# Optimization experiments

Hardware: AMD Instinct MI355X
Metric: run time of the kernel (lower is better)

## Reference

```python
import jax, jax.numpy as jnp
import numpy as np

N = 50000      # nodes
E = 800000     # edges
G = 256        # graphs in batch
D_IN = 128     # input_dim
H = 128        # node_hidden_dim
FC = 128       # fc_hidden_dim
OUT = 2        # out_dim
EPS = 1e-5


def _lin_init(key, fan_in, fan_out, bias=True):
    kw, kb = jax.random.split(key)
    w = jax.random.normal(kw, (fan_in, fan_out), jnp.float32) / np.sqrt(fan_in)
    if bias:
        b = jax.random.normal(kb, (fan_out,), jnp.float32) * 0.01
        return w, b
    return w


def setup_inputs() -> dict:
    key = jax.random.key(0)
    ks = jax.random.split(key, 16)
    x = jax.random.normal(ks[0], (N, D_IN), jnp.float32)
    edge_index = jax.random.randint(ks[1], (2, E), 0, N, jnp.int32)
    batch = jnp.sort(jax.random.randint(ks[2], (N,), 0, G, jnp.int32))
    edge_attr = jax.random.uniform(ks[3], (E, 1), jnp.float32)
    # GraphConv params: lin_rel (with bias) + lin_root (no bias)
    w_rel1, b_rel1 = _lin_init(ks[4], D_IN, H)
    w_root1 = _lin_init(ks[5], D_IN, H, bias=False)
    w_rel2, b_rel2 = _lin_init(ks[6], H, 2 * H)
    w_root2 = _lin_init(ks[7], H, 2 * H, bias=False)
    w_rel3, b_rel3 = _lin_init(ks[8], 2 * H, 3 * H)
    w_root3 = _lin_init(ks[9], 2 * H, 3 * H, bias=False)
    # BatchNorm affine params
    gamma1 = jnp.ones((H,), jnp.float32);      beta1 = jnp.zeros((H,), jnp.float32)
    gamma2 = jnp.ones((2 * H,), jnp.float32);  beta2 = jnp.zeros((2 * H,), jnp.float32)
    gamma3 = jnp.ones((3 * H,), jnp.float32);  beta3 = jnp.zeros((3 * H,), jnp.float32)
    # FC head: lin1 in = 3H+6H+9H = 18H
    w_lin1, b_lin1 = _lin_init(ks[10], 18 * H, FC)
    w_lin2, b_lin2 = _lin_init(ks[11], FC, OUT)
    w_lin3, b_lin3 = _lin_init(ks[12], OUT, OUT)
    return dict(x=x, edge_index=edge_index, batch=batch, edge_attr=edge_attr,
                w_rel1=w_rel1, b_rel1=b_rel1, w_root1=w_root1,
                w_rel2=w_rel2, b_rel2=b_rel2, w_root2=w_root2,
                w_rel3=w_rel3, b_rel3=b_rel3, w_root3=w_root3,
                gamma1=gamma1, beta1=beta1, gamma2=gamma2, beta2=beta2,
                gamma3=gamma3, beta3=beta3,
                w_lin1=w_lin1, b_lin1=b_lin1, w_lin2=w_lin2, b_lin2=b_lin2,
                w_lin3=w_lin3, b_lin3=b_lin3)


def _bn(h, gamma, beta):
    # training-mode BatchNorm1d over node axis
    mu = h.mean(0)
    var = h.var(0)
    return (h - mu) * jax.lax.rsqrt(var + EPS) * gamma + beta


def _gconv(h, src, dst, ew, w_rel, b_rel, w_root):
    # PyG GraphConv: lin_rel(sum_j ew_ij * x_j) + lin_root(x_i)
    agg = jax.ops.segment_sum(h[src] * ew[:, None], dst, num_segments=N)
    return agg @ w_rel + b_rel + h @ w_root


def _pool3(h, batch):
    # concat of global max / mean / add pooling per graph
    s = jax.ops.segment_sum(h, batch, num_segments=G)
    cnt = jax.ops.segment_sum(jnp.ones((h.shape[0], 1), h.dtype), batch, num_segments=G)
    mean = s / jnp.maximum(cnt, 1.0)
    m = jax.ops.segment_max(h, batch, num_segments=G)
    m = jnp.where(cnt > 0, m, 0.0)  # guard empty segments
    return jnp.concatenate([m, mean, s], axis=1)


def reference(x, edge_index, batch, edge_attr,
              w_rel1, b_rel1, w_root1, w_rel2, b_rel2, w_root2,
              w_rel3, b_rel3, w_root3,
              gamma1, beta1, gamma2, beta2, gamma3, beta3,
              w_lin1, b_lin1, w_lin2, b_lin2, w_lin3, b_lin3):
    ew = jnp.transpose(edge_attr, (1, 0))[0]            # [E]
    src, dst = edge_index[0], edge_index[1]
    h = _bn(jax.nn.leaky_relu(_gconv(x, src, dst, ew, w_rel1, b_rel1, w_root1)), gamma1, beta1)
    x1 = _pool3(h, batch)
    h = _bn(jax.nn.leaky_relu(_gconv(h, src, dst, ew, w_rel2, b_rel2, w_root2)), gamma2, beta2)
    x2 = _pool3(h, batch)
    h = _bn(jax.nn.leaky_relu(_gconv(h, src, dst, ew, w_rel3, b_rel3, w_root3)), gamma3, beta3)
    x3 = _pool3(h, batch)
    z = jnp.concatenate([x1, x2, x3], axis=1)           # [G, 18H]
    z = jax.nn.relu(z @ w_lin1 + b_lin1)                # dropout is identity in eval
    z = jax.nn.relu(z @ w_lin2 + b_lin2)
    return jax.nn.log_softmax(z @ w_lin3 + b_lin3, axis=-1)
```

## Files before the change

### kernel.cpp

```cpp
#include <hip/hip_runtime.h>
#include <cstdint>
#include <cstddef>

#define N_NODES 50000
#define M_PAD   50048
#define MB_TILES 391
#define N_EDGES 800000
#define N_GRAPH 256
#define Z_DIM   2304
#define NREP    16
#define POOL_TOT (N_GRAPH * (128 + 256 + 384))

static constexpr float LEAKY  = 0.01f;
static constexpr float BN_EPS = 1e-5f;

typedef short short8 __attribute__((ext_vector_type(8)));
typedef float floatx4 __attribute__((ext_vector_type(4)));
typedef const __attribute__((address_space(1))) unsigned int* gas_ptr;
typedef __attribute__((address_space(3))) unsigned int* las_ptr;
typedef unsigned long long ull;

__device__ __forceinline__ unsigned short f2b(float f) {
  union { float f; unsigned int u; } v; v.f = f;
  unsigned int u = v.u;
  unsigned int r = (u + 0x7FFFu + ((u >> 16) & 1u)) >> 16;
  return (unsigned short)r;
}
__device__ __forceinline__ float b2f(unsigned short h) {
  union { unsigned int u; float f; } v; v.u = ((unsigned int)h) << 16;
  return v.f;
}
__device__ __forceinline__ unsigned fkey(float x) {
  unsigned k = __float_as_uint(x);
  return k ^ ((k & 0x80000000u) ? 0xFFFFFFFFu : 0x80000000u);
}
__device__ __forceinline__ float kdec(unsigned k) {
  k ^= (k & 0x80000000u) ? 0x80000000u : 0xFFFFFFFFu;
  return __uint_as_float(k);
}


__global__ void init_all_kernel(int* __restrict__ cntR, int* __restrict__ gcnt,
                                float* __restrict__ sums_all,
                                unsigned* __restrict__ pmaxk, unsigned* __restrict__ pmink,
                                float* __restrict__ psumg) {
  const int i = blockIdx.x * blockDim.x + threadIdx.x;
  if (i < NREP * N_NODES) cntR[i] = 0;
  if (i < N_GRAPH) gcnt[i] = 0;
  if (i < 2 * (128 + 256 + 384)) sums_all[i] = 0.f;
  if (i < POOL_TOT) { pmaxk[i] = 0u; pmink[i] = 0xFFFFFFFFu; psumg[i] = 0.f; }
}


__global__ void hist_rep_kernel(const int* __restrict__ idx, int* __restrict__ cntR, int n) {
  int i = blockIdx.x * blockDim.x + threadIdx.x;
  if (i < n) {
    const int rep = blockIdx.x & (NREP - 1);
    atomicAdd(&cntR[rep * N_NODES + idx[i]], 1);
  }
}

__global__ void combine_kernel(int* __restrict__ cntR, int* __restrict__ deg, int n) {
  int d = blockIdx.x * blockDim.x + threadIdx.x;
  if (d >= n) return;
  int s = 0;
#pragma unroll
  for (int r = 0; r < NREP; ++r) {
    const int c = cntR[r * N_NODES + d];
    cntR[r * N_NODES + d] = s;
    s += c;
  }
  deg[d] = s;
}

__global__ __launch_bounds__(256) void scan1_kernel(const int* __restrict__ in,
                                                    int* __restrict__ out,
                                                    int* __restrict__ part, int n) {
  __shared__ int sm[256];
  const int t = threadIdx.x;
  const int base = blockIdx.x * 1024 + t * 4;
  int v0 = 0, v1 = 0, v2 = 0, v3 = 0;
  if (base + 3 < n) {
    int4 q = *(const int4*)(in + base);
    v0 = q.x; v1 = q.y; v2 = q.z; v3 = q.w;
  } else {
    if (base     < n) v0 = in[base];
    if (base + 1 < n) v1 = in[base + 1];
    if (base + 2 < n) v2 = in[base + 2];
  }
  const int tsum = v0 + v1 + v2 + v3;
  sm[t] = tsum;
  __syncthreads();
  for (int off = 1; off < 256; off <<= 1) {
    int x = (t >= off) ? sm[t - off] : 0;
    __syncthreads();
    sm[t] += x;
    __syncthreads();
  }
  const int excl = sm[t] - tsum;
  if (base     < n) out[base]     = excl;
  if (base + 1 < n) out[base + 1] = excl + v0;
  if (base + 2 < n) out[base + 2] = excl + v0 + v1;
  if (base + 3 < n) out[base + 3] = excl + v0 + v1 + v2;
  if (t == 255) part[blockIdx.x] = sm[255];
}

__global__ __launch_bounds__(256) void scan2_kernel(int* __restrict__ part, int nb,
                                                    int* __restrict__ total_out) {
  __shared__ int sm[256];
  const int t = threadIdx.x;
  const int v = (t < nb) ? part[t] : 0;
  sm[t] = v;
  __syncthreads();
  for (int off = 1; off < 256; off <<= 1) {
    int x = (t >= off) ? sm[t - off] : 0;
    __syncthreads();
    sm[t] += x;
    __syncthreads();
  }
  if (t < nb) part[t] = sm[t] - v;
  if (t == 255) *total_out = sm[255];
}

__global__ void scan3_cursor_kernel(int* __restrict__ out, const int* __restrict__ part,
                                    int* __restrict__ cntR, int n) {
  int i = blockIdx.x * blockDim.x + threadIdx.x;
  if (i >= n) return;
  const int rp = out[i] + part[i >> 10];
  out[i] = rp;
#pragma unroll
  for (int r = 0; r < NREP; ++r) cntR[r * N_NODES + i] += rp;
}

__global__ void bucket_kernel(const int* __restrict__ src, const int* __restrict__ dst,
                              const float* __restrict__ ew, int* __restrict__ cntR,
                              ull* __restrict__ epack, int E) {
  int e = blockIdx.x * blockDim.x + threadIdx.x;
  if (e < E) {
    const int rep = blockIdx.x & (NREP - 1);
    const int d = dst[e];
    const int p = atomicAdd(&cntR[rep * N_NODES + d], 1);
    epack[p] = ((ull)__float_as_uint(ew[e]) << 32) | (unsigned)src[e];
  }
}

__global__ __launch_bounds__(256) void hist_batch_kernel(const int* __restrict__ idx,
                                                         int* __restrict__ cnt, int n) {
  __shared__ int lh[N_GRAPH];
  lh[threadIdx.x] = 0;
  __syncthreads();
  int i = blockIdx.x * blockDim.x + threadIdx.x;
  if (i < n) atomicAdd(&lh[idx[i]], 1);
  __syncthreads();
  const int v = lh[threadIdx.x];
  if (v) atomicAdd(&cnt[threadIdx.x], v);
}

__global__ __launch_bounds__(256) void scan256_kernel(const int* __restrict__ cnt,
                                                      int* __restrict__ gptr) {
  __shared__ int sm[256];
  const int t = threadIdx.x;
  const int v = cnt[t];
  sm[t] = v;
  __syncthreads();
  for (int off = 1; off < 256; off <<= 1) {
    int x = (t >= off) ? sm[t - off] : 0;
    __syncthreads();
    sm[t] += x;
    __syncthreads();
  }
  gptr[t] = sm[t] - v;
  if (t == 255) gptr[256] = sm[255];
}


__global__ void cast_bf16_kernel(const float* __restrict__ in,
                                 unsigned short* __restrict__ out, int npair) {
  int i = blockIdx.x * blockDim.x + threadIdx.x;
  if (i >= npair) return;
  float2 v = *(const float2*)(in + 2 * (size_t)i);
  ((unsigned int*)out)[i] = (unsigned int)f2b(v.x) | ((unsigned int)f2b(v.y) << 16);
}

__global__ __launch_bounds__(256) void wt_build_kernel(
    const float* __restrict__ wrel, const float* __restrict__ wroot,
    const float* __restrict__ brel, const float* __restrict__ sums_prev,
    const float* __restrict__ gamma_prev, const float* __restrict__ beta_prev,
    unsigned short* __restrict__ wt, float* __restrict__ u, float* __restrict__ v,
    int K, int N) {
  __shared__ float redu[256];
  __shared__ float redv[256];
  const int n = blockIdx.x;
  const int K2 = 2 * K;
  const float inv_n = 1.f / (float)N_NODES;
  float us = 0.f, vs = 0.f;
  for (int k = threadIdx.x; k < K2; k += 256) {
    const int kk = (k < K) ? k : k - K;
    const float w = (k < K) ? wrel[(size_t)kk * N + n] : wroot[(size_t)kk * N + n];
    float sc = 1.f, sh = 0.f;
    if (sums_prev) {
      const float mu  = sums_prev[kk] * inv_n;
      const float var = sums_prev[K + kk] * inv_n - mu * mu;
      sc = rsqrtf(var + BN_EPS) * gamma_prev[kk];
      sh = beta_prev[kk] - mu * sc;
    }
    wt[(size_t)n * K2 + k] = f2b(w * sc);
    if (k < K) us += sh * w; else vs += sh * w;
  }
  redu[threadIdx.x] = us; redv[threadIdx.x] = vs;
  __syncthreads();
  for (int o = 128; o > 0; o >>= 1) {
    if (threadIdx.x < o) {
      redu[threadIdx.x] += redu[threadIdx.x + o];
      redv[threadIdx.x] += redv[threadIdx.x + o];
    }
    __syncthreads();
  }
  if (threadIdx.x == 0) { u[n] = redu[0]; v[n] = brel[n] + redv[0]; }
}


template <int D>
__global__ void agg_bf16_kernel(const unsigned short* __restrict__ h,
                                const int* __restrict__ rowptr,
                                const ull* __restrict__ epack,
                                unsigned short* __restrict__ agg,
                                float* __restrict__ degw_out) {
  int gid  = blockIdx.x * blockDim.x + threadIdx.x;
  int node = gid >> 6;
  int lane = threadIdx.x & 63;
  if (node >= N_NODES) return;
  const int beg = rowptr[node], end = rowptr[node + 1];
  constexpr int NP = D / 128;
  float acc0[NP], acc1[NP];
#pragma unroll
  for (int i = 0; i < NP; ++i) { acc0[i] = 0.f; acc1[i] = 0.f; }
  float wsum = 0.f;

  int p = beg;
  for (; p + 4 <= end; p += 4) {
    const ull p0 = epack[p],     p1 = epack[p + 1];
    const ull p2 = epack[p + 2], p3 = epack[p + 3];
    const int s0 = (int)(unsigned)p0, s1 = (int)(unsigned)p1;
    const int s2 = (int)(unsigned)p2, s3 = (int)(unsigned)p3;
    const float w0 = __uint_as_float((unsigned)(p0 >> 32));
    const float w1 = __uint_as_float((unsigned)(p1 >> 32));
    const float w2 = __uint_as_float((unsigned)(p2 >> 32));
    const float w3 = __uint_as_float((unsigned)(p3 >> 32));
    wsum += w0 + w1 + w2 + w3;
    const unsigned int* r0 = (const unsigned int*)(h + (size_t)s0 * D);
    const unsigned int* r1 = (const unsigned int*)(h + (size_t)s1 * D);
    const unsigned int* r2 = (const unsigned int*)(h + (size_t)s2 * D);
    const unsigned int* r3 = (const unsigned int*)(h + (size_t)s3 * D);
    unsigned int u0[NP], u1[NP], u2[NP], u3[NP];
#pragma unroll
    for (int i = 0; i < NP; ++i) {
      u0[i] = r0[lane + 64 * i];
      u1[i] = r1[lane + 64 * i];
      u2[i] = r2[lane + 64 * i];
      u3[i] = r3[lane + 64 * i];
    }
#pragma unroll
    for (int i = 0; i < NP; ++i) {
      acc0[i] += b2f((unsigned short)(u0[i] & 0xFFFF)) * w0
               + b2f((unsigned short)(u1[i] & 0xFFFF)) * w1
               + b2f((unsigned short)(u2[i] & 0xFFFF)) * w2
               + b2f((unsigned short)(u3[i] & 0xFFFF)) * w3;
      acc1[i] += b2f((unsigned short)(u0[i] >> 16)) * w0
               + b2f((unsigned short)(u1[i] >> 16)) * w1
               + b2f((unsigned short)(u2[i] >> 16)) * w2
               + b2f((unsigned short)(u3[i] >> 16)) * w3;
    }
  }
  for (; p < end; ++p) {
    const ull pk = epack[p];
    const int   s = (int)(unsigned)pk;
    const float w = __uint_as_float((unsigned)(pk >> 32));
    wsum += w;
    const unsigned int* row = (const unsigned int*)(h + (size_t)s * D);
#pragma unroll
    for (int i = 0; i < NP; ++i) {
      unsigned int uu = row[lane + 64 * i];
      acc0[i] += b2f((unsigned short)(uu & 0xFFFF)) * w;
      acc1[i] += b2f((unsigned short)(uu >> 16)) * w;
    }
  }
  unsigned int* o = (unsigned int*)(agg + (size_t)node * D);
#pragma unroll
  for (int i = 0; i < NP; ++i)
    o[lane + 64 * i] = (unsigned int)f2b(acc0[i]) | ((unsigned int)f2b(acc1[i]) << 16);
  if (degw_out != nullptr && lane == 0) degw_out[node] = wsum;
}


__global__ __launch_bounds__(256) void gemm_mfma_kernel(
    const unsigned short* __restrict__ Aagg, const unsigned short* __restrict__ Ah,
    const unsigned short* __restrict__ Wt,
    const float* __restrict__ u, const float* __restrict__ v,
    const float* __restrict__ degw,
    unsigned short* __restrict__ outH, float* __restrict__ sums,
    int M, int K, int N) {
  __shared__ unsigned short As[2][128 * 32];
  __shared__ unsigned short Bs[2][128 * 32];
  __shared__ float col_s[256];
  __shared__ float dws[128];

  const int NT = N >> 7;
  const int id = blockIdx.x;
  const int xcd = id & 7;
  const int q   = id >> 3;
  const int m_tile = (q / NT) * 8 + xcd;
  if (m_tile >= MB_TILES) return;
  const int m0 = m_tile * 128;
  const int n0 = (q % NT) * 128;

  const int t  = threadIdx.x;
  const int lane = t & 63;
  const int w    = t >> 6;
  const int wm   = (w & 1) * 64;
  const int wn   = (w >> 1) * 64;
  const int l16  = lane & 15;
  const int lq   = lane >> 4;
  const int K2   = 2 * K;

  const int lrow  = lane >> 2;
  const int lslot = lane & 3;

  col_s[t] = 0.f;
  if (t < 128) {
    const int m = m0 + t;
    dws[t] = (m < M) ? degw[m] : 0.f;
  }

  floatx4 acc[4][4];
#pragma unroll
  for (int i = 0; i < 4; ++i)
#pragma unroll
    for (int j = 0; j < 4; ++j) acc[i][j] = (floatx4){0.f, 0.f, 0.f, 0.f};

  for (int k0 = 0; k0 < K2; k0 += 64) {
    __syncthreads();
#pragma unroll
    for (int h = 0; h < 2; ++h) {
      const int kk = k0 + h * 32;
      const unsigned short* Asrc;
      int kbase;
      if (kk < K) { Asrc = Aagg; kbase = kk; } else { Asrc = Ah; kbase = kk - K; }
#pragma unroll
      for (int qq = 0; qq < 2; ++qq) {
        const int row = w * 32 + qq * 16 + lrow;
        const int gc  = (lslot ^ ((row >> 1) & 3)) * 8;
        const unsigned short* gA = Asrc + (size_t)(m0 + row) * K + kbase + gc;
        const unsigned short* gB = Wt + (size_t)(n0 + row) * K2 + kk + gc;
        __builtin_amdgcn_global_load_lds((gas_ptr)gA,
                                         (las_ptr)(As[h] + (w * 32 + qq * 16) * 32), 16, 0, 0);
        __builtin_amdgcn_global_load_lds((gas_ptr)gB,
                                         (las_ptr)(Bs[h] + (w * 32 + qq * 16) * 32), 16, 0, 0);
      }
    }
    __syncthreads();

#pragma unroll
    for (int h = 0; h < 2; ++h) {
      short8 af[4], bfr[4];
#pragma unroll
      for (int i = 0; i < 4; ++i) {
        const int r = wm + i * 16 + l16;
        af[i] = *(const short8*)(As[h] + r * 32 + (lq ^ ((r >> 1) & 3)) * 8);
      }
#pragma unroll
      for (int j = 0; j < 4; ++j) {
        const int r = wn + j * 16 + l16;
        bfr[j] = *(const short8*)(Bs[h] + r * 32 + (lq ^ ((r >> 1) & 3)) * 8);
      }
#pragma unroll
      for (int i = 0; i < 4; ++i)
#pragma unroll
        for (int j = 0; j < 4; ++j)
          acc[i][j] = __builtin_amdgcn_mfma_f32_16x16x32_bf16(af[i], bfr[j], acc[i][j], 0, 0, 0);
    }
  }

  float uu[4], vv[4];
#pragma unroll
  for (int j = 0; j < 4; ++j) {
    const int n = n0 + wn + j * 16 + l16;
    uu[j] = u[n]; vv[j] = v[n];
  }

  float ts[4]  = {0.f, 0.f, 0.f, 0.f};
  float tss[4] = {0.f, 0.f, 0.f, 0.f};
#pragma unroll
  for (int i = 0; i < 4; ++i) {
    const int lrow2 = wm + i * 16 + lq * 4;
#pragma unroll
    for (int j = 0; j < 4; ++j) {
      const int n = n0 + wn + j * 16 + l16;
#pragma unroll
      for (int r = 0; r < 4; ++r) {
        const int m = m0 + lrow2 + r;
        if (m < M) {
          float val = acc[i][j][r] + vv[j] + dws[lrow2 + r] * uu[j];
          val = val > 0.f ? val : LEAKY * val;
          outH[(size_t)m * N + n] = f2b(val);
          ts[j]  += val;
          tss[j] += val * val;
        }
      }
    }
  }
#pragma unroll
  for (int j = 0; j < 4; ++j) {
    float a = ts[j], b = tss[j];
    a += __shfl_xor(a, 16); a += __shfl_xor(a, 32);
    b += __shfl_xor(b, 16); b += __shfl_xor(b, 32);
    if (lq == 0) {
      const int ci = wn + j * 16 + l16;
      atomicAdd(&col_s[ci], a);
      atomicAdd(&col_s[128 + ci], b);
    }
  }
  __syncthreads();
  if (t < 128) {
    atomicAdd(&sums[n0 + t], col_s[t]);
    atomicAdd(&sums[N + n0 + t], col_s[128 + t]);
  }
}


__global__ void pool_bf16_kernel(const unsigned short* __restrict__ hp,
                                 const int* __restrict__ batch,
                                 unsigned* __restrict__ pmaxk, unsigned* __restrict__ pmink,
                                 float* __restrict__ psumg, int n, int C) {
  __shared__ int bs[64];
  const int tc = threadIdx.x;
  const int r0 = blockIdx.x * 64;
  const int r1 = min(n, r0 + 64);
  if (tc < 64 && r0 + tc < n) bs[tc] = batch[r0 + tc];
  __syncthreads();
  int cur_g = bs[0];
  float mx0 = -3.4e38f, mn0 = 3.4e38f, s0 = 0.f;
  float mx1 = -3.4e38f, mn1 = 3.4e38f, s1 = 0.f;
  for (int r = r0; r < r1; ++r) {
    const int g = bs[r - r0];
    if (g != cur_g) {
      const int c0 = 2 * tc;
      atomicMax(&pmaxk[(size_t)cur_g * C + c0], fkey(mx0));
      atomicMin(&pmink[(size_t)cur_g * C + c0], fkey(mn0));
      atomicAdd(&psumg[(size_t)cur_g * C + c0], s0);
      atomicMax(&pmaxk[(size_t)cur_g * C + c0 + 1], fkey(mx1));
      atomicMin(&pmink[(size_t)cur_g * C + c0 + 1], fkey(mn1));
      atomicAdd(&psumg[(size_t)cur_g * C + c0 + 1], s1);
      mx0 = -3.4e38f; mn0 = 3.4e38f; s0 = 0.f;
      mx1 = -3.4e38f; mn1 = 3.4e38f; s1 = 0.f;
      cur_g = g;
    }
    const unsigned uu = ((const unsigned*)(hp + (size_t)r * C))[tc];
    const float a = b2f((unsigned short)(uu & 0xFFFF));
    const float b = b2f((unsigned short)(uu >> 16));
    mx0 = fmaxf(mx0, a); mn0 = fminf(mn0, a); s0 += a;
    mx1 = fmaxf(mx1, b); mn1 = fminf(mn1, b); s1 += b;
  }
  const int c0 = 2 * tc;
  atomicMax(&pmaxk[(size_t)cur_g * C + c0], fkey(mx0));
  atomicMin(&pmink[(size_t)cur_g * C + c0], fkey(mn0));
  atomicAdd(&psumg[(size_t)cur_g * C + c0], s0);
  atomicMax(&pmaxk[(size_t)cur_g * C + c0 + 1], fkey(mx1));
  atomicMin(&pmink[(size_t)cur_g * C + c0 + 1], fkey(mn1));
  atomicAdd(&psumg[(size_t)cur_g * C + c0 + 1], s1);
}


__global__ void pool_finalize_kernel(const unsigned* __restrict__ pmaxk,
                                     const unsigned* __restrict__ pmink,
                                     const float* __restrict__ psumg,
                                     const float* __restrict__ sums,
                                     const float* __restrict__ gamma,
                                     const float* __restrict__ beta,
                                     const int* __restrict__ gptr,
                                     float* __restrict__ z, int C, int zoff) {
  int i = blockIdx.x * blockDim.x + threadIdx.x;
  if (i >= N_GRAPH * C) return;
  const int g = i / C, c = i % C;
  const int cnt = gptr[g + 1] - gptr[g];
  const float inv_n = 1.f / (float)N_NODES;
  const float mu  = sums[c] * inv_n;
  const float var = sums[C + c] * inv_n - mu * mu;
  const float sc  = rsqrtf(var + BN_EPS) * gamma[c];
  const float sh  = beta[c] - mu * sc;
  const float mx = kdec(pmaxk[i]);
  const float mn = kdec(pmink[i]);
  const float sm = psumg[i];
  const float zmax = (sc >= 0.f ? mx : mn) * sc + sh;
  const float zsum = sm * sc + (float)cnt * sh;
  float* zg = z + (size_t)g * Z_DIM + zoff;
  zg[c]         = (cnt > 0) ? zmax : 0.f;
  zg[C + c]     = zsum / (float)(cnt > 0 ? cnt : 1);
  zg[2 * C + c] = zsum;
}


__global__ __launch_bounds__(1024) void fc_kernel(const float* __restrict__ z,
                                                  const float* __restrict__ w1, const float* __restrict__ b1,
                                                  const float* __restrict__ w2, const float* __restrict__ b2,
                                                  const float* __restrict__ w3, const float* __restrict__ b3,
                                                  float* __restrict__ out) {
  __shared__ float zs[Z_DIM];
  __shared__ float part[8][128];
  __shared__ float h1s[128];
  __shared__ float red[128][2];
  __shared__ float y2[2];
  const int g  = blockIdx.x;
  const int t  = threadIdx.x;
  const int c  = t & 127;
  const int ks = t >> 7;
  for (int i = t; i < Z_DIM; i += 1024) zs[i] = z[(size_t)g * Z_DIM + i];
  __syncthreads();

  constexpr int KCH = Z_DIM / 8;
  const int k0 = ks * KCH;
  float acc = 0.f;
#pragma unroll 4
  for (int k = k0; k < k0 + KCH; ++k) acc += zs[k] * w1[(size_t)k * 128 + c];
  part[ks][c] = acc;
  __syncthreads();

  if (t < 128) {
    float s = b1[t];
#pragma unroll
    for (int i = 0; i < 8; ++i) s += part[i][t];
    h1s[t] = fmaxf(s, 0.f);
  }
  __syncthreads();
  if (t < 128) {
    red[t][0] = h1s[t] * w2[t * 2 + 0];
    red[t][1] = h1s[t] * w2[t * 2 + 1];
  }
  __syncthreads();
  if (t < 2) {
    float s = b2[t];
    for (int k = 0; k < 128; ++k) s += red[k][t];
    y2[t] = fmaxf(s, 0.f);
  }
  __syncthreads();
  if (t == 0) {
    const float z0 = y2[0] * w3[0] + y2[1] * w3[2] + b3[0];
    const float z1 = y2[0] * w3[1] + y2[1] * w3[3] + b3[1];
    const float m  = fmaxf(z0, z1);
    const float lse = m + logf(expf(z0 - m) + expf(z1 - m));
    out[g * 2 + 0] = z0 - lse;
    out[g * 2 + 1] = z1 - lse;
  }
}


extern "C" void kernel_launch(void* const* d_in, const int* in_sizes, int n_in,
                              void* d_out, int out_size, void* d_ws, size_t ws_size,
                              hipStream_t stream) {
  (void)in_sizes; (void)n_in; (void)out_size; (void)ws_size;
  const float* x        = (const float*)d_in[0];
  const int*   eidx     = (const int*)d_in[1];
  const int*   batch    = (const int*)d_in[2];
  const float* eattr    = (const float*)d_in[3];
  const float* w_rel1   = (const float*)d_in[4];
  const float* b_rel1   = (const float*)d_in[5];
  const float* w_root1  = (const float*)d_in[6];
  const float* w_rel2   = (const float*)d_in[7];
  const float* b_rel2   = (const float*)d_in[8];
  const float* w_root2  = (const float*)d_in[9];
  const float* w_rel3   = (const float*)d_in[10];
  const float* b_rel3   = (const float*)d_in[11];
  const float* w_root3  = (const float*)d_in[12];
  const float* gamma1   = (const float*)d_in[13];
  const float* beta1    = (const float*)d_in[14];
  const float* gamma2   = (const float*)d_in[15];
  const float* beta2    = (const float*)d_in[16];
  const float* gamma3   = (const float*)d_in[17];
  const float* beta3    = (const float*)d_in[18];
  const float* w_lin1   = (const float*)d_in[19];
  const float* b_lin1   = (const float*)d_in[20];
  const float* w_lin2   = (const float*)d_in[21];
  const float* b_lin2   = (const float*)d_in[22];
  const float* w_lin3   = (const float*)d_in[23];
  const float* b_lin3   = (const float*)d_in[24];

  const int* src = eidx;
  const int* dst = eidx + N_EDGES;
  float* outp = (float*)d_out;

  char* ws = (char*)d_ws;
  size_t off = 0;
  auto alloc = [&](size_t bytes) -> void* {
    void* p = ws + off;
    off += (bytes + 255) & ~(size_t)255;
    return p;
  };
  int*   rowptr = (int*)alloc((N_NODES + 1) * sizeof(int));
  int*   deg    = (int*)alloc(N_NODES * sizeof(int));
  int*   cntR   = (int*)alloc((size_t)NREP * N_NODES * sizeof(int));
  int*   gptr   = (int*)alloc((N_GRAPH + 1) * sizeof(int));
  int*   gcnt   = (int*)alloc(N_GRAPH * sizeof(int));
  int*   part   = (int*)alloc(256 * sizeof(int));
  ull*   epack  = (ull*)alloc((size_t)N_EDGES * sizeof(ull));
  float* degw   = (float*)alloc(N_NODES * sizeof(float));
  float* sums_all = (float*)alloc(2 * (128 + 256 + 384) * sizeof(float));
  float* zbuf   = (float*)alloc((size_t)N_GRAPH * Z_DIM * sizeof(float));
  unsigned* pmaxk = (unsigned*)alloc((size_t)POOL_TOT * 4);
  unsigned* pmink = (unsigned*)alloc((size_t)POOL_TOT * 4);
  float*    psumg = (float*)alloc((size_t)POOL_TOT * 4);
  unsigned short* xb   = (unsigned short*)alloc((size_t)M_PAD * 128 * 2);
  unsigned short* hp1  = (unsigned short*)alloc((size_t)M_PAD * 128 * 2);
  unsigned short* hp2  = (unsigned short*)alloc((size_t)M_PAD * 256 * 2);
  unsigned short* hp3  = (unsigned short*)alloc((size_t)M_PAD * 384 * 2);
  unsigned short* aggb = (unsigned short*)alloc((size_t)M_PAD * 256 * 2);
  unsigned short* wt1 = (unsigned short*)alloc((size_t)128 * 256 * 2);
  unsigned short* wt2 = (unsigned short*)alloc((size_t)256 * 256 * 2);
  unsigned short* wt3 = (unsigned short*)alloc((size_t)384 * 512 * 2);
  float* u1 = (float*)alloc(128 * sizeof(float));
  float* v1 = (float*)alloc(128 * sizeof(float));
  float* u2 = (float*)alloc(256 * sizeof(float));
  float* v2 = (float*)alloc(256 * sizeof(float));
  float* u3 = (float*)alloc(384 * sizeof(float));
  float* v3 = (float*)alloc(384 * sizeof(float));

  float* sums1 = sums_all;
  float* sums2 = sums_all + 2 * 128;
  float* sums3 = sums_all + 2 * (128 + 256);
  const int PO1 = 0, PO2 = N_GRAPH * 128, PO3 = N_GRAPH * (128 + 256);

  const int EB = (N_EDGES + 255) / 256;
  const int NB = (N_NODES + 255) / 256;
  const int RB = (N_NODES + 63) / 64;
  const int SB = (N_NODES + 1023) / 1024;

  init_all_kernel<<<(NREP * N_NODES + 255) / 256, 256, 0, stream>>>(
      cntR, gcnt, sums_all, pmaxk, pmink, psumg);

  hist_rep_kernel<<<EB, 256, 0, stream>>>(dst, cntR, N_EDGES);
  combine_kernel<<<NB, 256, 0, stream>>>(cntR, deg, N_NODES);
  scan1_kernel<<<SB, 256, 0, stream>>>(deg, rowptr, part, N_NODES);
  scan2_kernel<<<1, 256, 0, stream>>>(part, SB, rowptr + N_NODES);
  scan3_cursor_kernel<<<NB, 256, 0, stream>>>(rowptr, part, cntR, N_NODES);
  bucket_kernel<<<EB, 256, 0, stream>>>(src, dst, eattr, cntR, epack, N_EDGES);

  hist_batch_kernel<<<NB, 256, 0, stream>>>(batch, gcnt, N_NODES);
  scan256_kernel<<<1, 256, 0, stream>>>(gcnt, gptr);

  cast_bf16_kernel<<<(N_NODES * 128 / 2 + 255) / 256, 256, 0, stream>>>(x, xb, N_NODES * 128 / 2);
  wt_build_kernel<<<128, 256, 0, stream>>>(w_rel1, w_root1, b_rel1, nullptr, nullptr, nullptr,
                                           wt1, u1, v1, 128, 128);

  const int aggBlocks = (N_NODES * 64 + 255) / 256;

  agg_bf16_kernel<128><<<aggBlocks, 256, 0, stream>>>(xb, rowptr, epack, aggb, degw);
  gemm_mfma_kernel<<<392 * 1, 256, 0, stream>>>(aggb, xb, wt1, u1, v1, degw,
                                                hp1, sums1, N_NODES, 128, 128);
  pool_bf16_kernel<<<RB, 64, 0, stream>>>(hp1, batch, pmaxk + PO1, pmink + PO1, psumg + PO1,
                                          N_NODES, 128);
  pool_finalize_kernel<<<(N_GRAPH * 128 + 255) / 256, 256, 0, stream>>>(
      pmaxk + PO1, pmink + PO1, psumg + PO1, sums1, gamma1, beta1, gptr, zbuf, 128, 0);
  wt_build_kernel<<<256, 256, 0, stream>>>(w_rel2, w_root2, b_rel2, sums1, gamma1, beta1,
                                           wt2, u2, v2, 128, 256);

  agg_bf16_kernel<128><<<aggBlocks, 256, 0, stream>>>(hp1, rowptr, epack, aggb, nullptr);
  gemm_mfma_kernel<<<392 * 2, 256, 0, stream>>>(aggb, hp1, wt2, u2, v2, degw,
                                                hp2, sums2, N_NODES, 128, 256);
  pool_bf16_kernel<<<RB, 128, 0, stream>>>(hp2, batch, pmaxk + PO2, pmink + PO2, psumg + PO2,
                                           N_NODES, 256);
  pool_finalize_kernel<<<(N_GRAPH * 256 + 255) / 256, 256, 0, stream>>>(
      pmaxk + PO2, pmink + PO2, psumg + PO2, sums2, gamma2, beta2, gptr, zbuf, 256, 384);
  wt_build_kernel<<<384, 256, 0, stream>>>(w_rel3, w_root3, b_rel3, sums2, gamma2, beta2,
                                           wt3, u3, v3, 256, 384);

  agg_bf16_kernel<256><<<aggBlocks, 256, 0, stream>>>(hp2, rowptr, epack, aggb, nullptr);
  gemm_mfma_kernel<<<392 * 3, 256, 0, stream>>>(aggb, hp2, wt3, u3, v3, degw,
                                                hp3, sums3, N_NODES, 256, 384);
  pool_bf16_kernel<<<RB, 192, 0, stream>>>(hp3, batch, pmaxk + PO3, pmink + PO3, psumg + PO3,
                                           N_NODES, 384);
  pool_finalize_kernel<<<(N_GRAPH * 384 + 255) / 256, 256, 0, stream>>>(
      pmaxk + PO3, pmink + PO3, psumg + PO3, sums3, gamma3, beta3, gptr, zbuf, 384, 1152);

  fc_kernel<<<N_GRAPH, 1024, 0, stream>>>(zbuf, w_lin1, b_lin1, w_lin2, b_lin2, w_lin3, b_lin3,
                                          outp);
}
```

Measured before the change: 582.2 us.

## Fuse degree combine into scan, merge pool finalizes, shrink GEMM K-step

Folds the per-replica degree combine into the first scan kernel and merges the three per-layer pool finalize launches into one launch at the end. Together these remove three kernel launches. Separately, the MFMA GEMM drops its two-half LDS buffers and iterates K in steps of 32 instead of 64. That halves LDS use, which may raise occupancy, but doubles the number of barriers per tile. The fused scan now does strided 16-way loads per element instead of a coalesced int4 read, which may cost memory efficiency.

```diff
diff --git a/kernel.cpp b/kernel.cpp
--- a/kernel.cpp
+++ b/kernel.cpp
@@ -60,35 +60,28 @@
   }
 }
 
-__global__ void combine_kernel(int* __restrict__ cntR, int* __restrict__ deg, int n) {
-  int d = blockIdx.x * blockDim.x + threadIdx.x;
-  if (d >= n) return;
-  int s = 0;
-#pragma unroll
-  for (int r = 0; r < NREP; ++r) {
-    const int c = cntR[r * N_NODES + d];
-    cntR[r * N_NODES + d] = s;
-    s += c;
-  }
-  deg[d] = s;
-}
-
-__global__ __launch_bounds__(256) void scan1_kernel(const int* __restrict__ in,
-                                                    int* __restrict__ out,
-                                                    int* __restrict__ part, int n) {
+__global__ __launch_bounds__(256) void scan1_fused_kernel(int* __restrict__ cntR,
+                                                          int* __restrict__ out,
+                                                          int* __restrict__ part, int n) {
   __shared__ int sm[256];
   const int t = threadIdx.x;
   const int base = blockIdx.x * 1024 + t * 4;
-  int v0 = 0, v1 = 0, v2 = 0, v3 = 0;
-  if (base + 3 < n) {
-    int4 q = *(const int4*)(in + base);
-    v0 = q.x; v1 = q.y; v2 = q.z; v3 = q.w;
-  } else {
-    if (base     < n) v0 = in[base];
-    if (base + 1 < n) v1 = in[base + 1];
-    if (base + 2 < n) v2 = in[base + 2];
-  }
-  const int tsum = v0 + v1 + v2 + v3;
+  int v[4] = {0, 0, 0, 0};
+#pragma unroll
+  for (int j = 0; j < 4; ++j) {
+    const int d = base + j;
+    if (d < n) {
+      int s = 0;
+#pragma unroll
+      for (int r = 0; r < NREP; ++r) {
+        const int c = cntR[r * N_NODES + d];
+        cntR[r * N_NODES + d] = s;
+        s += c;
+      }
+      v[j] = s;
+    }
+  }
+  const int tsum = v[0] + v[1] + v[2] + v[3];
   sm[t] = tsum;
   __syncthreads();
   for (int off = 1; off < 256; off <<= 1) {
@@ -99,9 +92,9 @@
   }
   const int excl = sm[t] - tsum;
   if (base     < n) out[base]     = excl;
-  if (base + 1 < n) out[base + 1] = excl + v0;
-  if (base + 2 < n) out[base + 2] = excl + v0 + v1;
-  if (base + 3 < n) out[base + 3] = excl + v0 + v1 + v2;
+  if (base + 1 < n) out[base + 1] = excl + v[0];
+  if (base + 2 < n) out[base + 2] = excl + v[0] + v[1];
+  if (base + 3 < n) out[base + 3] = excl + v[0] + v[1] + v[2];
   if (t == 255) part[blockIdx.x] = sm[255];
 }
 
@@ -300,8 +293,8 @@
     const float* __restrict__ degw,
     unsigned short* __restrict__ outH, float* __restrict__ sums,
     int M, int K, int N) {
-  __shared__ unsigned short As[2][128 * 32];
-  __shared__ unsigned short Bs[2][128 * 32];
+  __shared__ unsigned short As[128 * 32];
+  __shared__ unsigned short Bs[128 * 32];
   __shared__ float col_s[256];
   __shared__ float dws[128];
 
@@ -338,47 +331,42 @@
 #pragma unroll
     for (int j = 0; j < 4; ++j) acc[i][j] = (floatx4){0.f, 0.f, 0.f, 0.f};
 
-  for (int k0 = 0; k0 < K2; k0 += 64) {
-    __syncthreads();
-#pragma unroll
-    for (int h = 0; h < 2; ++h) {
-      const int kk = k0 + h * 32;
-      const unsigned short* Asrc;
-      int kbase;
-      if (kk < K) { Asrc = Aagg; kbase = kk; } else { Asrc = Ah; kbase = kk - K; }
-#pragma unroll
-      for (int qq = 0; qq < 2; ++qq) {
-        const int row = w * 32 + qq * 16 + lrow;
-        const int gc  = (lslot ^ ((row >> 1) & 3)) * 8;
-        const unsigned short* gA = Asrc + (size_t)(m0 + row) * K + kbase + gc;
-        const unsigned short* gB = Wt + (size_t)(n0 + row) * K2 + kk + gc;
-        __builtin_amdgcn_global_load_lds((gas_ptr)gA,
-                                         (las_ptr)(As[h] + (w * 32 + qq * 16) * 32), 16, 0, 0);
-        __builtin_amdgcn_global_load_lds((gas_ptr)gB,
-                                         (las_ptr)(Bs[h] + (w * 32 + qq * 16) * 32), 16, 0, 0);
-      }
-    }
-    __syncthreads();
-
-#pragma unroll
-    for (int h = 0; h < 2; ++h) {
-      short8 af[4], bfr[4];
-#pragma unroll
-      for (int i = 0; i < 4; ++i) {
-        const int r = wm + i * 16 + l16;
-        af[i] = *(const short8*)(As[h] + r * 32 + (lq ^ ((r >> 1) & 3)) * 8);
-      }
-#pragma unroll
-      for (int j = 0; j < 4; ++j) {
-        const int r = wn + j * 16 + l16;
-        bfr[j] = *(const short8*)(Bs[h] + r * 32 + (lq ^ ((r >> 1) & 3)) * 8);
-      }
-#pragma unroll
-      for (int i = 0; i < 4; ++i)
-#pragma unroll
-        for (int j = 0; j < 4; ++j)
-          acc[i][j] = __builtin_amdgcn_mfma_f32_16x16x32_bf16(af[i], bfr[j], acc[i][j], 0, 0, 0);
-    }
+  for (int k0 = 0; k0 < K2; k0 += 32) {
+    const unsigned short* Asrc;
+    int kbase;
+    if (k0 < K) { Asrc = Aagg; kbase = k0; } else { Asrc = Ah; kbase = k0 - K; }
+
+    __syncthreads();
+#pragma unroll
+    for (int qq = 0; qq < 2; ++qq) {
+      const int row = w * 32 + qq * 16 + lrow;
+      const int gc  = (lslot ^ ((row >> 1) & 3)) * 8;
+      const unsigned short* gA = Asrc + (size_t)(m0 + row) * K + kbase + gc;
+      const unsigned short* gB = Wt + (size_t)(n0 + row) * K2 + k0 + gc;
+      __builtin_amdgcn_global_load_lds((gas_ptr)gA, (las_ptr)(As + (w * 32 + qq * 16) * 32),
+                                       16, 0, 0);
+      __builtin_amdgcn_global_load_lds((gas_ptr)gB, (las_ptr)(Bs + (w * 32 + qq * 16) * 32),
+                                       16, 0, 0);
+    }
+    __syncthreads();
+
+    short8 af[4], bfr[4];
+#pragma unroll
+    for (int i = 0; i < 4; ++i) {
+      const int r = wm + i * 16 + l16;
+      af[i] = *(const short8*)(As + r * 32 + (lq ^ ((r >> 1) & 3)) * 8);
+    }
+#pragma unroll
+    for (int j = 0; j < 4; ++j) {
+      const int r = wn + j * 16 + l16;
+      bfr[j] = *(const short8*)(Bs + r * 32 + (lq ^ ((r >> 1) & 3)) * 8);
+    }
+
+#pragma unroll
+    for (int i = 0; i < 4; ++i)
+#pragma unroll
+      for (int j = 0; j < 4; ++j)
+        acc[i][j] = __builtin_amdgcn_mfma_f32_16x16x32_bf16(af[i], bfr[j], acc[i][j], 0, 0, 0);
   }
 
   float uu[4], vv[4];
@@ -471,17 +459,30 @@
 }
 
 
-__global__ void pool_finalize_kernel(const unsigned* __restrict__ pmaxk,
-                                     const unsigned* __restrict__ pmink,
-                                     const float* __restrict__ psumg,
-                                     const float* __restrict__ sums,
-                                     const float* __restrict__ gamma,
-                                     const float* __restrict__ beta,
-                                     const int* __restrict__ gptr,
-                                     float* __restrict__ z, int C, int zoff) {
+__global__ void pool_finalize_all_kernel(const unsigned* __restrict__ pmaxk,
+                                         const unsigned* __restrict__ pmink,
+                                         const float* __restrict__ psumg,
+                                         const float* __restrict__ sums_all,
+                                         const float* __restrict__ gamma1, const float* __restrict__ beta1,
+                                         const float* __restrict__ gamma2, const float* __restrict__ beta2,
+                                         const float* __restrict__ gamma3, const float* __restrict__ beta3,
+                                         const int* __restrict__ gptr,
+                                         float* __restrict__ z) {
   int i = blockIdx.x * blockDim.x + threadIdx.x;
-  if (i >= N_GRAPH * C) return;
-  const int g = i / C, c = i % C;
+  if (i >= POOL_TOT) return;
+  int C, zoff, li;
+  const float *sums, *gamma, *beta;
+  if (i < N_GRAPH * 128) {
+    C = 128; zoff = 0; li = i;
+    sums = sums_all; gamma = gamma1; beta = beta1;
+  } else if (i < N_GRAPH * (128 + 256)) {
+    C = 256; zoff = 384; li = i - N_GRAPH * 128;
+    sums = sums_all + 2 * 128; gamma = gamma2; beta = beta2;
+  } else {
+    C = 384; zoff = 1152; li = i - N_GRAPH * (128 + 256);
+    sums = sums_all + 2 * (128 + 256); gamma = gamma3; beta = beta3;
+  }
+  const int g = li / C, c = li % C;
   const int cnt = gptr[g + 1] - gptr[g];
   const float inv_n = 1.f / (float)N_NODES;
   const float mu  = sums[c] * inv_n;
@@ -596,7 +597,6 @@
     return p;
   };
   int*   rowptr = (int*)alloc((N_NODES + 1) * sizeof(int));
-  int*   deg    = (int*)alloc(N_NODES * sizeof(int));
   int*   cntR   = (int*)alloc((size_t)NREP * N_NODES * sizeof(int));
   int*   gptr   = (int*)alloc((N_GRAPH + 1) * sizeof(int));
   int*   gcnt   = (int*)alloc(N_GRAPH * sizeof(int));
@@ -637,8 +637,7 @@
       cntR, gcnt, sums_all, pmaxk, pmink, psumg);
 
   hist_rep_kernel<<<EB, 256, 0, stream>>>(dst, cntR, N_EDGES);
-  combine_kernel<<<NB, 256, 0, stream>>>(cntR, deg, N_NODES);
-  scan1_kernel<<<SB, 256, 0, stream>>>(deg, rowptr, part, N_NODES);
+  scan1_fused_kernel<<<SB, 256, 0, stream>>>(cntR, rowptr, part, N_NODES);
   scan2_kernel<<<1, 256, 0, stream>>>(part, SB, rowptr + N_NODES);
   scan3_cursor_kernel<<<NB, 256, 0, stream>>>(rowptr, part, cntR, N_NODES);
   bucket_kernel<<<EB, 256, 0, stream>>>(src, dst, eattr, cntR, epack, N_EDGES);
@@ -657,8 +656,6 @@
                                                 hp1, sums1, N_NODES, 128, 128);
   pool_bf16_kernel<<<RB, 64, 0, stream>>>(hp1, batch, pmaxk + PO1, pmink + PO1, psumg + PO1,
                                           N_NODES, 128);
-  pool_finalize_kernel<<<(N_GRAPH * 128 + 255) / 256, 256, 0, stream>>>(
-      pmaxk + PO1, pmink + PO1, psumg + PO1, sums1, gamma1, beta1, gptr, zbuf, 128, 0);
   wt_build_kernel<<<256, 256, 0, stream>>>(w_rel2, w_root2, b_rel2, sums1, gamma1, beta1,
                                            wt2, u2, v2, 128, 256);
 
@@ -667,8 +664,6 @@
                                                 hp2, sums2, N_NODES, 128, 256);
   pool_bf16_kernel<<<RB, 128, 0, stream>>>(hp2, batch, pmaxk + PO2, pmink + PO2, psumg + PO2,
                                            N_NODES, 256);
-  pool_finalize_kernel<<<(N_GRAPH * 256 + 255) / 256, 256, 0, stream>>>(
-      pmaxk + PO2, pmink + PO2, psumg + PO2, sums2, gamma2, beta2, gptr, zbuf, 256, 384);
   wt_build_kernel<<<384, 256, 0, stream>>>(w_rel3, w_root3, b_rel3, sums2, gamma2, beta2,
                                            wt3, u3, v3, 256, 384);
 
@@ -677,9 +672,9 @@
                                                 hp3, sums3, N_NODES, 256, 384);
   pool_bf16_kernel<<<RB, 192, 0, stream>>>(hp3, batch, pmaxk + PO3, pmink + PO3, psumg + PO3,
                                            N_NODES, 384);
-  pool_finalize_kernel<<<(N_GRAPH * 384 + 255) / 256, 256, 0, stream>>>(
-      pmaxk + PO3, pmink + PO3, psumg + PO3, sums3, gamma3, beta3, gptr, zbuf, 384, 1152);
-
+
+  pool_finalize_all_kernel<<<(POOL_TOT + 255) / 256, 256, 0, stream>>>(
+      pmaxk, pmink, psumg, sums_all, gamma1, beta1, gamma2, beta2, gamma3, beta3, gptr, zbuf);
   fc_kernel<<<N_GRAPH, 1024, 0, stream>>>(zbuf, w_lin1, b_lin1, w_lin2, b_lin2, w_lin3, b_lin3,
                                           outp);
 }
```

New measurement: 577.0 us. No clear change (-0.9%).
